# Optimization experiments

Hardware: AMD Instinct MI355X
Metric: run time of the kernel (lower is better)

Reference implementation:

```python
import jax, jax.numpy as jnp
import numpy as np

B, T, C = 2, 2048, 1024
H = 16
HS = C // H  # head_size = 64


def setup_inputs() -> dict:
    key = jax.random.key(0)
    k1, k2, k3 = jax.random.split(key, 3)
    x = jax.random.normal(k1, (B, T, C), dtype=jnp.float32)
    # nn.Linear(n_embd, 3*n_embd): weight [3C, C], bias [3C]
    W = jax.random.normal(k2, (3 * C, C), dtype=jnp.float32) * (C ** -0.5)
    b = jax.random.normal(k3, (3 * C,), dtype=jnp.float32) * 0.02
    return {"x": x, "W": W, "b": b}


def reference(x, W, b):
    Bs, Ts, Cs = x.shape
    # fused QKV projection: [B,T,3C]
    qkv = x @ W.T + b
    qkv = qkv.reshape(Bs, Ts, 3, H, HS)
    q, k, v = jnp.moveaxis(qkv, 2, 0)          # each [B,T,H,HS]
    q = q.transpose(0, 2, 1, 3)                 # [B,H,T,HS]
    k = k.transpose(0, 2, 1, 3)
    v = v.transpose(0, 2, 1, 3)
    scale = HS ** -0.5
    wei = jnp.einsum('bhqd,bhkd->bhqk', q, k) * scale  # [B,H,T,T]
    causal = jnp.tril(jnp.ones((Ts, Ts), dtype=bool))
    wei = jnp.where(causal, wei, -jnp.inf)
    wei = jax.nn.softmax(wei, axis=-1)
    out = jnp.einsum('bhqk,bhkd->bhqd', wei, v)        # [B,H,T,HS]
    return out.transpose(0, 2, 1, 3).reshape(Bs, Ts, Cs)
```

## Files before the change

kernel.cpp:

```cpp
#include <hip/hip_runtime.h>
#include <hip/hip_bf16.h>

typedef __attribute__((ext_vector_type(8))) short bf16x8;
typedef __attribute__((ext_vector_type(4))) float f32x4;

#define BATCH 2
#define T_SEQ 2048
#define C_EMB 1024
#define NH 16
#define HS 64

__device__ __forceinline__ void gld_lds16(const __hip_bfloat16* g, void* l) {
    __builtin_amdgcn_global_load_lds((const __attribute__((address_space(1))) uint32_t*)g,
                                     (__attribute__((address_space(3))) uint32_t*)l, 16, 0, 0);
}

__global__ void cvt_f32_bf16(const float4* __restrict__ s0, ushort4* __restrict__ d0, int n40,
                             const float4* __restrict__ s1, ushort4* __restrict__ d1, int n41) {
    int i = blockIdx.x * blockDim.x + threadIdx.x;
    const float4* s; ushort4* d; int j;
    if (i < n40)            { s = s0; d = d0; j = i; }
    else if (i < n40 + n41) { s = s1; d = d1; j = i - n40; }
    else return;
    float4 v = s[j];
    ushort4 o;
    __hip_bfloat16 h;
    h = __float2bfloat16(v.x); o.x = *(ushort*)&h;
    h = __float2bfloat16(v.y); o.y = *(ushort*)&h;
    h = __float2bfloat16(v.z); o.z = *(ushort*)&h;
    h = __float2bfloat16(v.w); o.w = *(ushort*)&h;
    d[j] = o;
}

#define NT_K 16

__launch_bounds__(512, 2)
__global__ void qkv_gemm(const __hip_bfloat16* __restrict__ xb,
                         const __hip_bfloat16* __restrict__ wb,
                         const float* __restrict__ bias,
                         __hip_bfloat16* __restrict__ qo,
                         __hip_bfloat16* __restrict__ ko,
                         __hip_bfloat16* __restrict__ vto)
{
    __shared__ __align__(16) char smem[114688];
    __hip_bfloat16* ASB = (__hip_bfloat16*)smem;
    __hip_bfloat16* BSB = (__hip_bfloat16*)(smem + 65536);
    const int K = C_EMB;
    const int nTn = (3 * C_EMB) / 192;
    int bid = blockIdx.x;
    int wgid = (bid & 7) * 32 + (bid >> 3);
    int bm = wgid / nTn, bn = wgid % nTn;
    int m0 = bm * 256, n0 = bn * 192;
    int tid  = threadIdx.x;
    int lane = tid & 63, w = tid >> 6;
    int wr = w >> 2, wc = w & 3;
    int c = lane & 15, g = lane >> 4;
    int sr = lane >> 2;
    int sj = (lane & 3) ^ ((sr >> 1) & 3);
    int rchnk = (g ^ ((c >> 1) & 3)) << 4;

#define STAGE_A(kt, kh, buf) \
    { _Pragma("unroll") for (int i_ = 0; i_ < 2; ++i_) { \
        int r0_ = w * 32 + i_ * 16; \
        gld_lds16(&xb[(size_t)(m0 + r0_ + sr) * K + (kt) * 64 + (kh) * 32 + sj * 8], \
                  &ASB[((buf) * 2 + (kh)) * 8192 + r0_ * 32]); } }
#define STAGE_B(kt, kh, buf) \
    { if (w < 4) { \
        gld_lds16(&wb[(size_t)(n0 + w * 32 + sr) * K + (kt) * 64 + (kh) * 32 + sj * 8], \
                  &BSB[((buf) * 2 + (kh)) * 6144 + (w * 32) * 32]); \
        gld_lds16(&wb[(size_t)(n0 + w * 32 + 16 + sr) * K + (kt) * 64 + (kh) * 32 + sj * 8], \
                  &BSB[((buf) * 2 + (kh)) * 6144 + (w * 32 + 16) * 32]); \
      } else { \
        gld_lds16(&wb[(size_t)(n0 + 128 + (w - 4) * 16 + sr) * K + (kt) * 64 + (kh) * 32 + sj * 8], \
                  &BSB[((buf) * 2 + (kh)) * 6144 + (128 + (w - 4) * 16) * 32]); \
      } }

    f32x4 acc[8][3];
#pragma unroll
    for (int mi = 0; mi < 8; ++mi)
#pragma unroll
        for (int ni = 0; ni < 3; ++ni)
            acc[mi][ni] = (f32x4){0.f, 0.f, 0.f, 0.f};

    STAGE_A(0, 0, 0); STAGE_B(0, 0, 0);
    STAGE_A(0, 1, 0); STAGE_B(0, 1, 0);
    STAGE_A(1, 0, 1); STAGE_B(1, 0, 1);
    if (w < 4) asm volatile("s_waitcnt vmcnt(4)" ::: "memory");
    else       asm volatile("s_waitcnt vmcnt(3)" ::: "memory");
    __builtin_amdgcn_s_barrier();

    for (int t = 0; t < NT_K; ++t) {
        int buf = t & 1;
#pragma unroll
        for (int ks = 0; ks < 2; ++ks) {
            const __hip_bfloat16* AL = &ASB[(buf * 2 + ks) * 8192];
            const __hip_bfloat16* BL = &BSB[(buf * 2 + ks) * 6144];
            bf16x8 af[8], bfr[3];
#pragma unroll
            for (int mi = 0; mi < 8; ++mi)
                af[mi] = *(const bf16x8*)((const char*)AL + (wr * 128 + mi * 16 + c) * 64 + rchnk);
#pragma unroll
            for (int ni = 0; ni < 3; ++ni)
                bfr[ni] = *(const bf16x8*)((const char*)BL + (wc * 48 + ni * 16 + c) * 64 + rchnk);
            if (ks == 0) {
                if (t + 1 < NT_K) { STAGE_A(t + 1, 1, buf ^ 1); STAGE_B(t + 1, 1, buf ^ 1); }
            } else {
                if (t + 2 < NT_K) { STAGE_A(t + 2, 0, buf); STAGE_B(t + 2, 0, buf); }
            }
            __builtin_amdgcn_s_barrier();
            asm volatile("s_waitcnt lgkmcnt(0)" ::: "memory");
            __builtin_amdgcn_s_setprio(1);
#pragma unroll
            for (int mi = 0; mi < 8; ++mi)
#pragma unroll
                for (int ni = 0; ni < 3; ++ni)
                    acc[mi][ni] = __builtin_amdgcn_mfma_f32_16x16x32_bf16(af[mi], bfr[ni], acc[mi][ni], 0, 0, 0);
            __builtin_amdgcn_s_setprio(0);
            if (ks == 1) {
                if (t + 2 < NT_K) {
                    if (w < 4) asm volatile("s_waitcnt vmcnt(4)" ::: "memory");
                    else       asm volatile("s_waitcnt vmcnt(3)" ::: "memory");
                } else {
                    asm volatile("s_waitcnt vmcnt(0)" ::: "memory");
                }
            }
            __builtin_amdgcn_s_barrier();
        }
    }
#undef STAGE_A
#undef STAGE_B

    const float QSCALE = 0.125f * 1.44269504088896340736f;
    __syncthreads();
    int b = m0 >> 11;
    int t0 = (m0 & (T_SEQ - 1)) + wr * 128;
#pragma unroll
    for (int ni = 0; ni < 3; ++ni) {
        int nb = n0 + wc * 48 + ni * 16;
        int s = nb >> 10;
        int h = (nb >> 6) & (NH - 1);
        float bv = bias[nb + c];
        if (s < 2) {
            __hip_bfloat16* dst = (s == 0) ? qo : ko;
            float scale = (s == 0) ? QSCALE : 1.0f;
            int dd = (nb & 63) + c;
            size_t bhb = (size_t)(b * NH + h) * T_SEQ;
#pragma unroll
            for (int mi = 0; mi < 8; ++mi) {
#pragma unroll
                for (int r = 0; r < 4; ++r) {
                    int tt = t0 + mi * 16 + g * 4 + r;
                    dst[(bhb + tt) * HS + dd] = __float2bfloat16((acc[mi][ni][r] + bv) * scale);
                }
            }
        } else {
            int dbase = nb & 63;
            char* scr = smem + (w * 3 + ni) * 4096;
#pragma unroll
            for (int mi = 0; mi < 8; ++mi) {
#pragma unroll
                for (int r = 0; r < 4; ++r) {
                    int m = mi * 16 + g * 4 + r;
                    __hip_bfloat16 hv = __float2bfloat16(acc[mi][ni][r] + bv);
                    *(ushort*)(scr + c * 256 + ((((m >> 3) ^ c) & 15) << 4) + (m & 7) * 2) = *(ushort*)&hv;
                }
            }
            size_t bh = (size_t)(b * NH + h);
#pragma unroll
            for (int p = 0; p < 4; ++p) {
                int d = p * 4 + g;
                bf16x8 vv = *(bf16x8*)(scr + d * 256 + (((c ^ d) & 15) << 4));
                *(bf16x8*)(&vto[(bh * HS + dbase + d) * T_SEQ + t0 + c * 8]) = vv;
            }
        }
    }
}

__launch_bounds__(256, 4)
__global__ void attn_fwd(const __hip_bfloat16* __restrict__ qb,
                         const __hip_bfloat16* __restrict__ kb,
                         const __hip_bfloat16* __restrict__ vtb,
                         float* __restrict__ out)
{
    __shared__ __align__(16) char smem[40960];

    int idx = blockIdx.x;
    int bh = idx & 31;
    int qt = 31 - (idx >> 5);
    int w  = threadIdx.x >> 6;
    int lane = threadIdx.x & 63;
    int c = lane & 15, g = lane >> 4;
    char* p_strip = smem + 32768 + w * 2048;

    const __hip_bfloat16* Qp = qb  + (size_t)bh * T_SEQ * HS;
    const __hip_bfloat16* Kp = kb  + (size_t)bh * T_SEQ * HS;
    const __hip_bfloat16* Vp = vtb + (size_t)bh * HS * T_SEQ;
    int b = bh >> 4, h = bh & (NH - 1);

    int srow = lane >> 3;
    int scol = ((lane & 7) ^ srow) << 3;
    int swz  = (c & 7) << 4;
    int krow0 = w * 16 + srow;
    int krow1 = w * 16 + 8 + srow;
    int qw = qt * 64 + w * 16;
    int ntile = qt + 1;

    bf16x8 qf[2];
    qf[0] = *(const bf16x8*)(&Qp[(size_t)(qw + c) * HS + g * 8]);
    qf[1] = *(const bf16x8*)(&Qp[(size_t)(qw + c) * HS + 32 + g * 8]);

    f32x4 oacc[4];
#pragma unroll
    for (int i = 0; i < 4; ++i) oacc[i] = (f32x4){0.f, 0.f, 0.f, 0.f};
    float lrow = 0.f;

#define ATT_STAGE(t_, buf_) { \
    int k0_ = (t_) * 64; \
    char* kb_ = smem + (buf_) * 8192; \
    char* vb_ = smem + 16384 + (buf_) * 8192; \
    gld_lds16(&Kp[(size_t)(k0_ + krow0) * HS + scol],  kb_ + (w * 16) * 128); \
    gld_lds16(&Kp[(size_t)(k0_ + krow1) * HS + scol],  kb_ + (w * 16 + 8) * 128); \
    gld_lds16(&Vp[(size_t)krow0 * T_SEQ + k0_ + scol], vb_ + (w * 16) * 128); \
    gld_lds16(&Vp[(size_t)krow1 * T_SEQ + k0_ + scol], vb_ + (w * 16 + 8) * 128); }

    ATT_STAGE(0, 0);

    for (int tix = 0; tix < ntile; ++tix) {
        int cur = tix & 1;
        asm volatile("s_waitcnt vmcnt(0)" ::: "memory");
        __builtin_amdgcn_s_barrier();
        if (tix + 1 < ntile) ATT_STAGE(tix + 1, cur ^ 1);

        bool diag = (tix == ntile - 1);
        const char* KL = smem + cur * 8192;
        const char* VL = smem + 16384 + cur * 8192;

        f32x4 sacc[4];
#pragma unroll
        for (int i = 0; i < 4; ++i) sacc[i] = (f32x4){0.f, 0.f, 0.f, 0.f};
        __builtin_amdgcn_s_setprio(1);
#pragma unroll
        for (int ks = 0; ks < 2; ++ks)
#pragma unroll
            for (int kc = 0; kc < 4; ++kc)
                if (!diag || kc <= w) {
                    int rr = kc * 16 + c;
                    int colB = (ks * 64 + g * 16) ^ swz;
                    bf16x8 kf = *(const bf16x8*)(KL + rr * 128 + colB);
                    sacc[kc] = __builtin_amdgcn_mfma_f32_16x16x32_bf16(kf, qf[ks], sacc[kc], 0, 0, 0);
                }
        __builtin_amdgcn_s_setprio(0);

#pragma unroll
        for (int kc = 0; kc < 4; ++kc) {
            float p0, p1, p2, p3;
            if (!diag) {
                p0 = __builtin_amdgcn_exp2f(sacc[kc][0]);
                p1 = __builtin_amdgcn_exp2f(sacc[kc][1]);
                p2 = __builtin_amdgcn_exp2f(sacc[kc][2]);
                p3 = __builtin_amdgcn_exp2f(sacc[kc][3]);
            } else {
                int kbase = kc * 16 + g * 4;
                int lim = w * 16 + c;
                p0 = (kc <= w && kbase + 0 <= lim) ? __builtin_amdgcn_exp2f(sacc[kc][0]) : 0.f;
                p1 = (kc <= w && kbase + 1 <= lim) ? __builtin_amdgcn_exp2f(sacc[kc][1]) : 0.f;
                p2 = (kc <= w && kbase + 2 <= lim) ? __builtin_amdgcn_exp2f(sacc[kc][2]) : 0.f;
                p3 = (kc <= w && kbase + 3 <= lim) ? __builtin_amdgcn_exp2f(sacc[kc][3]) : 0.f;
            }
            lrow += (p0 + p1) + (p2 + p3);
            unsigned lo = ((__builtin_bit_cast(unsigned, p0) + 0x8000u) >> 16) |
                          ((__builtin_bit_cast(unsigned, p1) + 0x8000u) & 0xffff0000u);
            unsigned hi = ((__builtin_bit_cast(unsigned, p2) + 0x8000u) >> 16) |
                          ((__builtin_bit_cast(unsigned, p3) + 0x8000u) & 0xffff0000u);
            int gran = ((kc * 2 + (g >> 1)) ^ (c & 7)) << 4;
            *(uint2*)(p_strip + c * 128 + gran + ((g & 1) << 3)) = make_uint2(lo, hi);
        }

        int ksm = diag ? ((w >= 2) ? 2 : 1) : 2;
        __builtin_amdgcn_s_setprio(1);
#pragma unroll
        for (int ks = 0; ks < 2; ++ks) {
            if (ks >= ksm) break;
            int pgran = ((ks * 4 + g) ^ (c & 7)) << 4;
            bf16x8 pf = *(bf16x8*)(p_strip + c * 128 + pgran);
#pragma unroll
            for (int d16 = 0; d16 < 4; ++d16) {
                int dr = d16 * 16 + c;
                int colB = (ks * 64 + g * 16) ^ swz;
                bf16x8 vf = *(const bf16x8*)(VL + dr * 128 + colB);
                oacc[d16] = __builtin_amdgcn_mfma_f32_16x16x32_bf16(vf, pf, oacc[d16], 0, 0, 0);
            }
        }
        __builtin_amdgcn_s_setprio(0);
    }

    float v = lrow;
    v += __shfl_xor(v, 16, 64);
    v += __shfl_xor(v, 32, 64);
    float linv = 1.0f / v;
    float* orow = &out[((size_t)(b * T_SEQ + qw + c)) * C_EMB + h * HS + g * 4];
#pragma unroll
    for (int d16 = 0; d16 < 4; ++d16) {
        float4 st;
        st.x = oacc[d16][0] * linv;
        st.y = oacc[d16][1] * linv;
        st.z = oacc[d16][2] * linv;
        st.w = oacc[d16][3] * linv;
        *(float4*)(&orow[d16 * 16]) = st;
    }
#undef ATT_STAGE
}

extern "C" void kernel_launch(void* const* d_in, const int* in_sizes, int n_in,
                              void* d_out, int out_size, void* d_ws, size_t ws_size,
                              hipStream_t stream) {
    const float* x    = (const float*)d_in[0];
    const float* W    = (const float*)d_in[1];
    const float* bias = (const float*)d_in[2];
    float* out = (float*)d_out;

    char* ws = (char*)d_ws;
    __hip_bfloat16* xb  = (__hip_bfloat16*)(ws);
    __hip_bfloat16* wb  = (__hip_bfloat16*)(ws + (8u  << 20));
    __hip_bfloat16* qo  = (__hip_bfloat16*)(ws + (14u << 20));
    __hip_bfloat16* ko  = (__hip_bfloat16*)(ws + (22u << 20));
    __hip_bfloat16* vto = (__hip_bfloat16*)(ws + (30u << 20));

    int n4x = BATCH * T_SEQ * C_EMB / 4;
    int n4w = 3 * C_EMB * C_EMB / 4;
    int n4  = n4x + n4w;
    cvt_f32_bf16<<<(n4 + 255) / 256, 256, 0, stream>>>(
        (const float4*)x, (ushort4*)xb, n4x,
        (const float4*)W, (ushort4*)wb, n4w);

    int gemm_grid = (BATCH * T_SEQ / 256) * (3 * C_EMB / 192);
    qkv_gemm<<<gemm_grid, 512, 0, stream>>>(xb, wb, bias, qo, ko, vto);

    attn_fwd<<<1024, 256, 0, stream>>>(qo, ko, vto, out);
}
```

Baseline: 78.09 us.

## Enlarge attention query tile to 128 rows with two query groups per wave

Each attention block now handles 128 query rows instead of 64, with each wave computing two 16-row query groups that share the K and V fragments read from LDS. This halves the grid and the number of K/V tile loads per query row, aiming to cut global and LDS traffic per unit of MFMA work. Waves whose diagonal tile is earlier skip later tiles, which leaves some waves idle on the final tile. Register and LDS use grow, and launch bounds drop to 2 blocks per CU.

```diff
diff --git a/kernel.cpp b/kernel.cpp
--- a/kernel.cpp
+++ b/kernel.cpp
@@ -176,21 +176,21 @@
     }
 }
 
-__launch_bounds__(256, 4)
+__launch_bounds__(256, 2)
 __global__ void attn_fwd(const __hip_bfloat16* __restrict__ qb,
                          const __hip_bfloat16* __restrict__ kb,
                          const __hip_bfloat16* __restrict__ vtb,
                          float* __restrict__ out)
 {
-    __shared__ __align__(16) char smem[40960];
+    __shared__ __align__(16) char smem[49152];
 
     int idx = blockIdx.x;
     int bh = idx & 31;
-    int qt = 31 - (idx >> 5);
+    int qt = 15 - (idx >> 5);
     int w  = threadIdx.x >> 6;
     int lane = threadIdx.x & 63;
     int c = lane & 15, g = lane >> 4;
-    char* p_strip = smem + 32768 + w * 2048;
+    char* p_strip = smem + 32768 + w * 4096;
 
     const __hip_bfloat16* Qp = qb  + (size_t)bh * T_SEQ * HS;
     const __hip_bfloat16* Kp = kb  + (size_t)bh * T_SEQ * HS;
@@ -202,17 +202,24 @@
     int swz  = (c & 7) << 4;
     int krow0 = w * 16 + srow;
     int krow1 = w * 16 + 8 + srow;
-    int qw = qt * 64 + w * 16;
-    int ntile = qt + 1;
-
-    bf16x8 qf[2];
-    qf[0] = *(const bf16x8*)(&Qp[(size_t)(qw + c) * HS + g * 8]);
-    qf[1] = *(const bf16x8*)(&Qp[(size_t)(qw + c) * HS + 32 + g * 8]);
-
-    f32x4 oacc[4];
-#pragma unroll
-    for (int i = 0; i < 4; ++i) oacc[i] = (f32x4){0.f, 0.f, 0.f, 0.f};
-    float lrow = 0.f;
+    int qw = qt * 128 + w * 32;
+    int ntile = 2 * qt + 2;
+    int mydiag = 2 * qt + (w >> 1);
+    int wh = w & 1;
+
+    bf16x8 qf[2][2];
+#pragma unroll
+    for (int ks = 0; ks < 2; ++ks)
+#pragma unroll
+        for (int qg = 0; qg < 2; ++qg)
+            qf[ks][qg] = *(const bf16x8*)(&Qp[(size_t)(qw + qg * 16 + c) * HS + ks * 32 + g * 8]);
+
+    f32x4 oacc[2][4];
+#pragma unroll
+    for (int qg = 0; qg < 2; ++qg)
+#pragma unroll
+        for (int i = 0; i < 4; ++i) oacc[qg][i] = (f32x4){0.f, 0.f, 0.f, 0.f};
+    float lrow[2] = {0.f, 0.f};
 
 #define ATT_STAGE(t_, buf_) { \
     int k0_ = (t_) * 64; \
@@ -231,82 +238,97 @@
         __builtin_amdgcn_s_barrier();
         if (tix + 1 < ntile) ATT_STAGE(tix + 1, cur ^ 1);
 
-        bool diag = (tix == ntile - 1);
-        const char* KL = smem + cur * 8192;
-        const char* VL = smem + 16384 + cur * 8192;
-
-        f32x4 sacc[4];
-#pragma unroll
-        for (int i = 0; i < 4; ++i) sacc[i] = (f32x4){0.f, 0.f, 0.f, 0.f};
-        __builtin_amdgcn_s_setprio(1);
-#pragma unroll
-        for (int ks = 0; ks < 2; ++ks)
-#pragma unroll
-            for (int kc = 0; kc < 4; ++kc)
-                if (!diag || kc <= w) {
-                    int rr = kc * 16 + c;
+        if (tix <= mydiag) {
+            bool diag = (tix == mydiag);
+            const char* KL = smem + cur * 8192;
+            const char* VL = smem + 16384 + cur * 8192;
+
+            f32x4 sacc[2][4];
+#pragma unroll
+            for (int qg = 0; qg < 2; ++qg)
+#pragma unroll
+                for (int i = 0; i < 4; ++i) sacc[qg][i] = (f32x4){0.f, 0.f, 0.f, 0.f};
+            __builtin_amdgcn_s_setprio(1);
+#pragma unroll
+            for (int ks = 0; ks < 2; ++ks)
+#pragma unroll
+                for (int kc = 0; kc < 4; ++kc)
+                    if (!diag || kc <= wh * 2 + 1) {
+                        int rr = kc * 16 + c;
+                        int colB = (ks * 64 + g * 16) ^ swz;
+                        bf16x8 kf = *(const bf16x8*)(KL + rr * 128 + colB);
+#pragma unroll
+                        for (int qg = 0; qg < 2; ++qg)
+                            if (!diag || kc <= wh * 2 + qg)
+                                sacc[qg][kc] = __builtin_amdgcn_mfma_f32_16x16x32_bf16(kf, qf[ks][qg], sacc[qg][kc], 0, 0, 0);
+                    }
+            __builtin_amdgcn_s_setprio(0);
+
+#pragma unroll
+            for (int qg = 0; qg < 2; ++qg) {
+#pragma unroll
+                for (int kc = 0; kc < 4; ++kc) {
+                    float p0, p1, p2, p3;
+                    if (!diag) {
+                        p0 = __builtin_amdgcn_exp2f(sacc[qg][kc][0]);
+                        p1 = __builtin_amdgcn_exp2f(sacc[qg][kc][1]);
+                        p2 = __builtin_amdgcn_exp2f(sacc[qg][kc][2]);
+                        p3 = __builtin_amdgcn_exp2f(sacc[qg][kc][3]);
+                    } else {
+                        int kbase = kc * 16 + g * 4;
+                        int lim = wh * 32 + qg * 16 + c;
+                        p0 = (kbase + 0 <= lim) ? __builtin_amdgcn_exp2f(sacc[qg][kc][0]) : 0.f;
+                        p1 = (kbase + 1 <= lim) ? __builtin_amdgcn_exp2f(sacc[qg][kc][1]) : 0.f;
+                        p2 = (kbase + 2 <= lim) ? __builtin_amdgcn_exp2f(sacc[qg][kc][2]) : 0.f;
+                        p3 = (kbase + 3 <= lim) ? __builtin_amdgcn_exp2f(sacc[qg][kc][3]) : 0.f;
+                    }
+                    lrow[qg] += (p0 + p1) + (p2 + p3);
+                    unsigned lo = ((__builtin_bit_cast(unsigned, p0) + 0x8000u) >> 16) |
+                                  ((__builtin_bit_cast(unsigned, p1) + 0x8000u) & 0xffff0000u);
+                    unsigned hi = ((__builtin_bit_cast(unsigned, p2) + 0x8000u) >> 16) |
+                                  ((__builtin_bit_cast(unsigned, p3) + 0x8000u) & 0xffff0000u);
+                    int gran = ((kc * 2 + (g >> 1)) ^ (c & 7)) << 4;
+                    *(uint2*)(p_strip + (qg * 16 + c) * 128 + gran + ((g & 1) << 3)) = make_uint2(lo, hi);
+                }
+            }
+
+            int ksm = diag ? (wh ? 2 : 1) : 2;
+            __builtin_amdgcn_s_setprio(1);
+#pragma unroll
+            for (int ks = 0; ks < 2; ++ks) {
+                if (ks >= ksm) break;
+                int pgran = ((ks * 4 + g) ^ (c & 7)) << 4;
+                bf16x8 pf0 = *(bf16x8*)(p_strip + c * 128 + pgran);
+                bf16x8 pf1 = *(bf16x8*)(p_strip + (16 + c) * 128 + pgran);
+#pragma unroll
+                for (int d16 = 0; d16 < 4; ++d16) {
+                    int dr = d16 * 16 + c;
                     int colB = (ks * 64 + g * 16) ^ swz;
-                    bf16x8 kf = *(const bf16x8*)(KL + rr * 128 + colB);
-                    sacc[kc] = __builtin_amdgcn_mfma_f32_16x16x32_bf16(kf, qf[ks], sacc[kc], 0, 0, 0);
-                }
-        __builtin_amdgcn_s_setprio(0);
-
-#pragma unroll
-        for (int kc = 0; kc < 4; ++kc) {
-            float p0, p1, p2, p3;
-            if (!diag) {
-                p0 = __builtin_amdgcn_exp2f(sacc[kc][0]);
-                p1 = __builtin_amdgcn_exp2f(sacc[kc][1]);
-                p2 = __builtin_amdgcn_exp2f(sacc[kc][2]);
-                p3 = __builtin_amdgcn_exp2f(sacc[kc][3]);
-            } else {
-                int kbase = kc * 16 + g * 4;
-                int lim = w * 16 + c;
-                p0 = (kc <= w && kbase + 0 <= lim) ? __builtin_amdgcn_exp2f(sacc[kc][0]) : 0.f;
-                p1 = (kc <= w && kbase + 1 <= lim) ? __builtin_amdgcn_exp2f(sacc[kc][1]) : 0.f;
-                p2 = (kc <= w && kbase + 2 <= lim) ? __builtin_amdgcn_exp2f(sacc[kc][2]) : 0.f;
-                p3 = (kc <= w && kbase + 3 <= lim) ? __builtin_amdgcn_exp2f(sacc[kc][3]) : 0.f;
-            }
-            lrow += (p0 + p1) + (p2 + p3);
-            unsigned lo = ((__builtin_bit_cast(unsigned, p0) + 0x8000u) >> 16) |
-                          ((__builtin_bit_cast(unsigned, p1) + 0x8000u) & 0xffff0000u);
-            unsigned hi = ((__builtin_bit_cast(unsigned, p2) + 0x8000u) >> 16) |
-                          ((__builtin_bit_cast(unsigned, p3) + 0x8000u) & 0xffff0000u);
-            int gran = ((kc * 2 + (g >> 1)) ^ (c & 7)) << 4;
-            *(uint2*)(p_strip + c * 128 + gran + ((g & 1) << 3)) = make_uint2(lo, hi);
+                    bf16x8 vf = *(const bf16x8*)(VL + dr * 128 + colB);
+                    oacc[0][d16] = __builtin_amdgcn_mfma_f32_16x16x32_bf16(vf, pf0, oacc[0][d16], 0, 0, 0);
+                    oacc[1][d16] = __builtin_amdgcn_mfma_f32_16x16x32_bf16(vf, pf1, oacc[1][d16], 0, 0, 0);
+                }
+            }
+            __builtin_amdgcn_s_setprio(0);
         }
-
-        int ksm = diag ? ((w >= 2) ? 2 : 1) : 2;
-        __builtin_amdgcn_s_setprio(1);
-#pragma unroll
-        for (int ks = 0; ks < 2; ++ks) {
-            if (ks >= ksm) break;
-            int pgran = ((ks * 4 + g) ^ (c & 7)) << 4;
-            bf16x8 pf = *(bf16x8*)(p_strip + c * 128 + pgran);
-#pragma unroll
-            for (int d16 = 0; d16 < 4; ++d16) {
-                int dr = d16 * 16 + c;
-                int colB = (ks * 64 + g * 16) ^ swz;
-                bf16x8 vf = *(const bf16x8*)(VL + dr * 128 + colB);
-                oacc[d16] = __builtin_amdgcn_mfma_f32_16x16x32_bf16(vf, pf, oacc[d16], 0, 0, 0);
-            }
+    }
+
+#pragma unroll
+    for (int qg = 0; qg < 2; ++qg) {
+        float v = lrow[qg];
+        v += __shfl_xor(v, 16, 64);
+        v += __shfl_xor(v, 32, 64);
+        float linv = 1.0f / v;
+        float* orow = &out[((size_t)(b * T_SEQ + qw + qg * 16 + c)) * C_EMB + h * HS + g * 4];
+#pragma unroll
+        for (int d16 = 0; d16 < 4; ++d16) {
+            float4 st;
+            st.x = oacc[qg][d16][0] * linv;
+            st.y = oacc[qg][d16][1] * linv;
+            st.z = oacc[qg][d16][2] * linv;
+            st.w = oacc[qg][d16][3] * linv;
+            *(float4*)(&orow[d16 * 16]) = st;
         }
-        __builtin_amdgcn_s_setprio(0);
-    }
-
-    float v = lrow;
-    v += __shfl_xor(v, 16, 64);
-    v += __shfl_xor(v, 32, 64);
-    float linv = 1.0f / v;
-    float* orow = &out[((size_t)(b * T_SEQ + qw + c)) * C_EMB + h * HS + g * 4];
-#pragma unroll
-    for (int d16 = 0; d16 < 4; ++d16) {
-        float4 st;
-        st.x = oacc[d16][0] * linv;
-        st.y = oacc[d16][1] * linv;
-        st.z = oacc[d16][2] * linv;
-        st.w = oacc[d16][3] * linv;
-        *(float4*)(&orow[d16 * 16]) = st;
     }
 #undef ATT_STAGE
 }
@@ -336,5 +358,5 @@
     int gemm_grid = (BATCH * T_SEQ / 256) * (3 * C_EMB / 192);
     qkv_gemm<<<gemm_grid, 512, 0, stream>>>(xb, wb, bias, qo, ko, vto);
 
-    attn_fwd<<<1024, 256, 0, stream>>>(qo, ko, vto, out);
-}
+    attn_fwd<<<512, 256, 0, stream>>>(qo, ko, vto, out);
+}
```

Result: slower. 88.87 us (+13.8%).

## Interleave LDS fragment loads and global staging with MFMA halves in QKV GEMM

Applied to the files above, without the earlier changes.

The QKV projection main loop now loads A fragments in two halves of four. The A and B global-to-LDS staging is spread between the two MFMA groups, so memory issue overlaps with compute. The mid-step barrier and explicit lgkmcnt wait are dropped. The vmcnt threshold is raised so more prefetch loads stay in flight. The goal is to cut stalls from serialized LDS reads and barriers, at the cost of relying on tighter wait-count bookkeeping for correctness.

```diff
diff --git a/kernel.cpp b/kernel.cpp
--- a/kernel.cpp
+++ b/kernel.cpp
@@ -74,6 +74,8 @@
         gld_lds16(&wb[(size_t)(n0 + 128 + (w - 4) * 16 + sr) * K + (kt) * 64 + (kh) * 32 + sj * 8], \
                   &BSB[((buf) * 2 + (kh)) * 6144 + (128 + (w - 4) * 16) * 32]); \
       } }
+#define WAIT_STEADY() { if (w < 4) asm volatile("s_waitcnt vmcnt(8)" ::: "memory"); \
+                        else       asm volatile("s_waitcnt vmcnt(6)" ::: "memory"); }
 
     f32x4 acc[8][3];
 #pragma unroll
@@ -85,8 +87,7 @@
     STAGE_A(0, 0, 0); STAGE_B(0, 0, 0);
     STAGE_A(0, 1, 0); STAGE_B(0, 1, 0);
     STAGE_A(1, 0, 1); STAGE_B(1, 0, 1);
-    if (w < 4) asm volatile("s_waitcnt vmcnt(4)" ::: "memory");
-    else       asm volatile("s_waitcnt vmcnt(3)" ::: "memory");
+    WAIT_STEADY();
     __builtin_amdgcn_s_barrier();
 
     for (int t = 0; t < NT_K; ++t) {
@@ -95,40 +96,45 @@
         for (int ks = 0; ks < 2; ++ks) {
             const __hip_bfloat16* AL = &ASB[(buf * 2 + ks) * 8192];
             const __hip_bfloat16* BL = &BSB[(buf * 2 + ks) * 6144];
-            bf16x8 af[8], bfr[3];
-#pragma unroll
-            for (int mi = 0; mi < 8; ++mi)
-                af[mi] = *(const bf16x8*)((const char*)AL + (wr * 128 + mi * 16 + c) * 64 + rchnk);
+            bf16x8 bfr[3];
 #pragma unroll
             for (int ni = 0; ni < 3; ++ni)
                 bfr[ni] = *(const bf16x8*)((const char*)BL + (wc * 48 + ni * 16 + c) * 64 + rchnk);
-            if (ks == 0) {
-                if (t + 1 < NT_K) { STAGE_A(t + 1, 1, buf ^ 1); STAGE_B(t + 1, 1, buf ^ 1); }
-            } else {
-                if (t + 2 < NT_K) { STAGE_A(t + 2, 0, buf); STAGE_B(t + 2, 0, buf); }
-            }
-            __builtin_amdgcn_s_barrier();
-            asm volatile("s_waitcnt lgkmcnt(0)" ::: "memory");
+            bf16x8 af[4];
+#pragma unroll
+            for (int mi = 0; mi < 4; ++mi)
+                af[mi] = *(const bf16x8*)((const char*)AL + (wr * 128 + mi * 16 + c) * 64 + rchnk);
+            if (ks == 0) { if (t + 1 < NT_K) STAGE_A(t + 1, 1, buf ^ 1); }
+            else         { if (t + 2 < NT_K) STAGE_A(t + 2, 0, buf); }
             __builtin_amdgcn_s_setprio(1);
 #pragma unroll
-            for (int mi = 0; mi < 8; ++mi)
+            for (int mi = 0; mi < 4; ++mi)
 #pragma unroll
                 for (int ni = 0; ni < 3; ++ni)
                     acc[mi][ni] = __builtin_amdgcn_mfma_f32_16x16x32_bf16(af[mi], bfr[ni], acc[mi][ni], 0, 0, 0);
             __builtin_amdgcn_s_setprio(0);
-            if (ks == 1) {
-                if (t + 2 < NT_K) {
-                    if (w < 4) asm volatile("s_waitcnt vmcnt(4)" ::: "memory");
-                    else       asm volatile("s_waitcnt vmcnt(3)" ::: "memory");
-                } else {
-                    asm volatile("s_waitcnt vmcnt(0)" ::: "memory");
-                }
-            }
+            bf16x8 af2[4];
+#pragma unroll
+            for (int mi = 0; mi < 4; ++mi)
+                af2[mi] = *(const bf16x8*)((const char*)AL + (wr * 128 + (mi + 4) * 16 + c) * 64 + rchnk);
+            if (ks == 0) { if (t + 1 < NT_K) STAGE_B(t + 1, 1, buf ^ 1); }
+            else         { if (t + 2 < NT_K) STAGE_B(t + 2, 0, buf); }
+            __builtin_amdgcn_s_setprio(1);
+#pragma unroll
+            for (int mi = 0; mi < 4; ++mi)
+#pragma unroll
+                for (int ni = 0; ni < 3; ++ni)
+                    acc[mi + 4][ni] = __builtin_amdgcn_mfma_f32_16x16x32_bf16(af2[mi], bfr[ni], acc[mi + 4][ni], 0, 0, 0);
+            __builtin_amdgcn_s_setprio(0);
+            bool staged = (ks == 0) ? (t + 1 < NT_K) : (t + 2 < NT_K);
+            if (staged) { WAIT_STEADY(); }
+            else        { asm volatile("s_waitcnt vmcnt(0)" ::: "memory"); }
             __builtin_amdgcn_s_barrier();
         }
     }
 #undef STAGE_A
 #undef STAGE_B
+#undef WAIT_STEADY
 
     const float QSCALE = 0.125f * 1.44269504088896340736f;
     __syncthreads();
```

Result: no change. 77.02 us (-1.4%).

## Fuse fp32-to-bf16 conversion into QKV GEMM tile loading via register staging

Applied to the files above, without the earlier changes.

Removes the separate conversion kernel and has the GEMM read fp32 x and W directly into registers, convert them with v_cvt_pk_bf16_f32, and write the bf16 tiles to LDS. This drops a kernel launch and a round trip of bf16 copies through global memory. The price is a switch from async global_load_lds to register-staged loads, which means more VGPRs, twice the global read bytes per tile, and a changed pipeline schedule. The attention kernel's manual bf16 rounding is also replaced by the packed conversion instruction.

```diff
diff --git a/kernel.cpp b/kernel.cpp
--- a/kernel.cpp
+++ b/kernel.cpp
@@ -15,28 +15,26 @@
                                      (__attribute__((address_space(3))) uint32_t*)l, 16, 0, 0);
 }
 
-__global__ void cvt_f32_bf16(const float4* __restrict__ s0, ushort4* __restrict__ d0, int n40,
-                             const float4* __restrict__ s1, ushort4* __restrict__ d1, int n41) {
-    int i = blockIdx.x * blockDim.x + threadIdx.x;
-    const float4* s; ushort4* d; int j;
-    if (i < n40)            { s = s0; d = d0; j = i; }
-    else if (i < n40 + n41) { s = s1; d = d1; j = i - n40; }
-    else return;
-    float4 v = s[j];
-    ushort4 o;
-    __hip_bfloat16 h;
-    h = __float2bfloat16(v.x); o.x = *(ushort*)&h;
-    h = __float2bfloat16(v.y); o.y = *(ushort*)&h;
-    h = __float2bfloat16(v.z); o.z = *(ushort*)&h;
-    h = __float2bfloat16(v.w); o.w = *(ushort*)&h;
-    d[j] = o;
+__device__ __forceinline__ unsigned pk_bf16(float a, float b) {
+    unsigned r;
+    asm("v_cvt_pk_bf16_f32 %0, %1, %2" : "=v"(r) : "v"(a), "v"(b));
+    return r;
+}
+
+__device__ __forceinline__ void pack_store(char* dst, float4 a, float4 b) {
+    uint4 u;
+    u.x = pk_bf16(a.x, a.y);
+    u.y = pk_bf16(a.z, a.w);
+    u.z = pk_bf16(b.x, b.y);
+    u.w = pk_bf16(b.z, b.w);
+    *(uint4*)dst = u;
 }
 
 #define NT_K 16
 
 __launch_bounds__(512, 2)
-__global__ void qkv_gemm(const __hip_bfloat16* __restrict__ xb,
-                         const __hip_bfloat16* __restrict__ wb,
+__global__ void qkv_gemm(const float* __restrict__ xf,
+                         const float* __restrict__ wf,
                          const float* __restrict__ bias,
                          __hip_bfloat16* __restrict__ qo,
                          __hip_bfloat16* __restrict__ ko,
@@ -45,7 +43,6 @@
     __shared__ __align__(16) char smem[114688];
     __hip_bfloat16* ASB = (__hip_bfloat16*)smem;
     __hip_bfloat16* BSB = (__hip_bfloat16*)(smem + 65536);
-    const int K = C_EMB;
     const int nTn = (3 * C_EMB) / 192;
     int bid = blockIdx.x;
     int wgid = (bid & 7) * 32 + (bid >> 3);
@@ -56,24 +53,34 @@
     int wr = w >> 2, wc = w & 3;
     int c = lane & 15, g = lane >> 4;
     int sr = lane >> 2;
-    int sj = (lane & 3) ^ ((sr >> 1) & 3);
+    int j  = lane & 3;
+    int pc = j ^ ((sr >> 1) & 3);
     int rchnk = (g ^ ((c >> 1) & 3)) << 4;
 
-#define STAGE_A(kt, kh, buf) \
-    { _Pragma("unroll") for (int i_ = 0; i_ < 2; ++i_) { \
-        int r0_ = w * 32 + i_ * 16; \
-        gld_lds16(&xb[(size_t)(m0 + r0_ + sr) * K + (kt) * 64 + (kh) * 32 + sj * 8], \
-                  &ASB[((buf) * 2 + (kh)) * 8192 + r0_ * 32]); } }
-#define STAGE_B(kt, kh, buf) \
-    { if (w < 4) { \
-        gld_lds16(&wb[(size_t)(n0 + w * 32 + sr) * K + (kt) * 64 + (kh) * 32 + sj * 8], \
-                  &BSB[((buf) * 2 + (kh)) * 6144 + (w * 32) * 32]); \
-        gld_lds16(&wb[(size_t)(n0 + w * 32 + 16 + sr) * K + (kt) * 64 + (kh) * 32 + sj * 8], \
-                  &BSB[((buf) * 2 + (kh)) * 6144 + (w * 32 + 16) * 32]); \
-      } else { \
-        gld_lds16(&wb[(size_t)(n0 + 128 + (w - 4) * 16 + sr) * K + (kt) * 64 + (kh) * 32 + sj * 8], \
-                  &BSB[((buf) * 2 + (kh)) * 6144 + (128 + (w - 4) * 16) * 32]); \
-      } }
+#define LOAD_AB(kt, kh, pa_, pb_) { \
+    int col_ = (kt) * 64 + (kh) * 32 + j * 8; \
+    _Pragma("unroll") for (int i_ = 0; i_ < 2; ++i_) { \
+        const float* s_ = &xf[(size_t)(m0 + w * 32 + i_ * 16 + sr) * 1024 + col_]; \
+        pa_[2 * i_] = *(const float4*)s_; pa_[2 * i_ + 1] = *(const float4*)(s_ + 4); } \
+    if (w < 4) { \
+        _Pragma("unroll") for (int i_ = 0; i_ < 2; ++i_) { \
+            const float* s_ = &wf[(size_t)(n0 + w * 32 + i_ * 16 + sr) * 1024 + col_]; \
+            pb_[2 * i_] = *(const float4*)s_; pb_[2 * i_ + 1] = *(const float4*)(s_ + 4); } \
+    } else { \
+        const float* s_ = &wf[(size_t)(n0 + 128 + (w - 4) * 16 + sr) * 1024 + col_]; \
+        pb_[0] = *(const float4*)s_; pb_[1] = *(const float4*)(s_ + 4); } }
+
+#define WRITE_AB(tb_, pa_, pb_) { \
+    _Pragma("unroll") for (int i_ = 0; i_ < 2; ++i_) \
+        pack_store((char*)&ASB[(tb_) * 8192 + (w * 32 + i_ * 16 + sr) * 32 + pc * 8], \
+                   pa_[2 * i_], pa_[2 * i_ + 1]); \
+    if (w < 4) { \
+        _Pragma("unroll") for (int i_ = 0; i_ < 2; ++i_) \
+            pack_store((char*)&BSB[(tb_) * 6144 + (w * 32 + i_ * 16 + sr) * 32 + pc * 8], \
+                       pb_[2 * i_], pb_[2 * i_ + 1]); \
+    } else { \
+        pack_store((char*)&BSB[(tb_) * 6144 + (128 + (w - 4) * 16 + sr) * 32 + pc * 8], \
+                   pb_[0], pb_[1]); } }
 
     f32x4 acc[8][3];
 #pragma unroll
@@ -82,12 +89,14 @@
         for (int ni = 0; ni < 3; ++ni)
             acc[mi][ni] = (f32x4){0.f, 0.f, 0.f, 0.f};
 
-    STAGE_A(0, 0, 0); STAGE_B(0, 0, 0);
-    STAGE_A(0, 1, 0); STAGE_B(0, 1, 0);
-    STAGE_A(1, 0, 1); STAGE_B(1, 0, 1);
-    if (w < 4) asm volatile("s_waitcnt vmcnt(4)" ::: "memory");
-    else       asm volatile("s_waitcnt vmcnt(3)" ::: "memory");
-    __builtin_amdgcn_s_barrier();
+    float4 s0a[4], s0b[4], s1a[4], s1b[4];
+    int tb_s0 = 0, tb_s1 = 0;
+    bool v_s0 = false, v_s1 = false;
+
+    LOAD_AB(0, 0, s0a, s0b); WRITE_AB(0, s0a, s0b);
+    LOAD_AB(0, 1, s0a, s0b); WRITE_AB(1, s0a, s0b);
+    LOAD_AB(1, 0, s1a, s1b); tb_s1 = 2; v_s1 = true;
+    __syncthreads();
 
     for (int t = 0; t < NT_K; ++t) {
         int buf = t & 1;
@@ -95,20 +104,20 @@
         for (int ks = 0; ks < 2; ++ks) {
             const __hip_bfloat16* AL = &ASB[(buf * 2 + ks) * 8192];
             const __hip_bfloat16* BL = &BSB[(buf * 2 + ks) * 6144];
-            bf16x8 af[8], bfr[3];
+            bf16x8 bfr[3], af[8];
+#pragma unroll
+            for (int ni = 0; ni < 3; ++ni)
+                bfr[ni] = *(const bf16x8*)((const char*)BL + (wc * 48 + ni * 16 + c) * 64 + rchnk);
 #pragma unroll
             for (int mi = 0; mi < 8; ++mi)
                 af[mi] = *(const bf16x8*)((const char*)AL + (wr * 128 + mi * 16 + c) * 64 + rchnk);
-#pragma unroll
-            for (int ni = 0; ni < 3; ++ni)
-                bfr[ni] = *(const bf16x8*)((const char*)BL + (wc * 48 + ni * 16 + c) * 64 + rchnk);
             if (ks == 0) {
-                if (t + 1 < NT_K) { STAGE_A(t + 1, 1, buf ^ 1); STAGE_B(t + 1, 1, buf ^ 1); }
+                if (t + 1 < NT_K) { LOAD_AB(t + 1, 1, s0a, s0b); tb_s0 = ((t + 1) & 1) * 2 + 1; v_s0 = true; }
+                else v_s0 = false;
             } else {
-                if (t + 2 < NT_K) { STAGE_A(t + 2, 0, buf); STAGE_B(t + 2, 0, buf); }
-            }
-            __builtin_amdgcn_s_barrier();
-            asm volatile("s_waitcnt lgkmcnt(0)" ::: "memory");
+                if (t + 2 < NT_K) { LOAD_AB(t + 2, 0, s1a, s1b); tb_s1 = ((t + 2) & 1) * 2; v_s1 = true; }
+                else v_s1 = false;
+            }
             __builtin_amdgcn_s_setprio(1);
 #pragma unroll
             for (int mi = 0; mi < 8; ++mi)
@@ -116,19 +125,14 @@
                 for (int ni = 0; ni < 3; ++ni)
                     acc[mi][ni] = __builtin_amdgcn_mfma_f32_16x16x32_bf16(af[mi], bfr[ni], acc[mi][ni], 0, 0, 0);
             __builtin_amdgcn_s_setprio(0);
-            if (ks == 1) {
-                if (t + 2 < NT_K) {
-                    if (w < 4) asm volatile("s_waitcnt vmcnt(4)" ::: "memory");
-                    else       asm volatile("s_waitcnt vmcnt(3)" ::: "memory");
-                } else {
-                    asm volatile("s_waitcnt vmcnt(0)" ::: "memory");
-                }
-            }
+            if (ks == 0) { if (v_s1) WRITE_AB(tb_s1, s1a, s1b); }
+            else         { if (v_s0) WRITE_AB(tb_s0, s0a, s0b); }
+            asm volatile("s_waitcnt lgkmcnt(0)" ::: "memory");
             __builtin_amdgcn_s_barrier();
         }
     }
-#undef STAGE_A
-#undef STAGE_B
+#undef LOAD_AB
+#undef WRITE_AB
 
     const float QSCALE = 0.125f * 1.44269504088896340736f;
     __syncthreads();
@@ -268,10 +272,8 @@
                 p3 = (kc <= w && kbase + 3 <= lim) ? __builtin_amdgcn_exp2f(sacc[kc][3]) : 0.f;
             }
             lrow += (p0 + p1) + (p2 + p3);
-            unsigned lo = ((__builtin_bit_cast(unsigned, p0) + 0x8000u) >> 16) |
-                          ((__builtin_bit_cast(unsigned, p1) + 0x8000u) & 0xffff0000u);
-            unsigned hi = ((__builtin_bit_cast(unsigned, p2) + 0x8000u) >> 16) |
-                          ((__builtin_bit_cast(unsigned, p3) + 0x8000u) & 0xffff0000u);
+            unsigned lo = pk_bf16(p0, p1);
+            unsigned hi = pk_bf16(p2, p3);
             int gran = ((kc * 2 + (g >> 1)) ^ (c & 7)) << 4;
             *(uint2*)(p_strip + c * 128 + gran + ((g & 1) << 3)) = make_uint2(lo, hi);
         }
@@ -320,21 +322,12 @@
     float* out = (float*)d_out;
 
     char* ws = (char*)d_ws;
-    __hip_bfloat16* xb  = (__hip_bfloat16*)(ws);
-    __hip_bfloat16* wb  = (__hip_bfloat16*)(ws + (8u  << 20));
     __hip_bfloat16* qo  = (__hip_bfloat16*)(ws + (14u << 20));
     __hip_bfloat16* ko  = (__hip_bfloat16*)(ws + (22u << 20));
     __hip_bfloat16* vto = (__hip_bfloat16*)(ws + (30u << 20));
 
-    int n4x = BATCH * T_SEQ * C_EMB / 4;
-    int n4w = 3 * C_EMB * C_EMB / 4;
-    int n4  = n4x + n4w;
-    cvt_f32_bf16<<<(n4 + 255) / 256, 256, 0, stream>>>(
-        (const float4*)x, (ushort4*)xb, n4x,
-        (const float4*)W, (ushort4*)wb, n4w);
-
     int gemm_grid = (BATCH * T_SEQ / 256) * (3 * C_EMB / 192);
-    qkv_gemm<<<gemm_grid, 512, 0, stream>>>(xb, wb, bias, qo, ko, vto);
+    qkv_gemm<<<gemm_grid, 512, 0, stream>>>(x, W, bias, qo, ko, vto);
 
     attn_fwd<<<1024, 256, 0, stream>>>(qo, ko, vto, out);
 }
```

New measurement: 74.14 us (median of 2 runs). 5.1% less time.
